# Kernel tuning notes

Measured on AMD Instinct MI355X. Metric: run time of the kernel, lower is better.

The kernel has to match this reference:

```python
import jax, jax.numpy as jnp
import numpy as np
from jax import lax

IN_PLANES = 64
OUT_PLANES = 128
NSAMPLE = 16
BN_EPS = 1e-5


def setup_inputs() -> dict:
    key = jax.random.key(0)
    k1, k2, k3 = jax.random.split(key, 3)
    B, N = 8, 8192
    xyz = jax.random.normal(k1, (B, N, 3), jnp.float32)
    feature = jax.random.normal(k2, (B, N, IN_PLANES), jnp.float32)
    W = jax.random.normal(k3, (OUT_PLANES, IN_PLANES), jnp.float32) * (1.0 / np.sqrt(IN_PLANES))
    gamma = jnp.ones((OUT_PLANES,), jnp.float32)
    beta = jnp.zeros((OUT_PLANES,), jnp.float32)
    return {"xyz": xyz, "feature": feature, "W": W, "gamma": gamma, "beta": beta, "npoint": 2048}


def farthest_point_sample(xyz, npoint):
    # xyz: [B, N, 3] -> centroids: [B, npoint] int32. Deterministic start at index 0
    # (torch version uses a random start; math is otherwise identical).
    B, N, _ = xyz.shape

    def step(carry, _):
        distance, farthest = carry  # [B,N], [B]
        centroid = jnp.take_along_axis(xyz, farthest[:, None, None], axis=1)  # [B,1,3]
        dist = jnp.sum((xyz - centroid) ** 2, axis=-1)  # [B,N]
        distance = jnp.minimum(distance, dist)
        new_far = jnp.argmax(distance, axis=-1).astype(jnp.int32)
        return (distance, new_far), farthest

    init = (jnp.full((B, N), 1e10, xyz.dtype), jnp.zeros((B,), jnp.int32))
    _, cents = lax.scan(step, init, None, length=npoint)  # [npoint, B]
    return cents.T  # [B, npoint]


def knn_point(nsample, xyz, new_xyz):
    # squared pairwise distances [B, M, N], then k smallest
    d = (-2.0 * jnp.einsum('bmc,bnc->bmn', new_xyz, xyz)
         + jnp.sum(new_xyz ** 2, -1)[:, :, None]
         + jnp.sum(xyz ** 2, -1)[:, None, :])
    _, idx = lax.top_k(-d, nsample)  # [B, M, nsample]
    return idx


def _forward(xyz, feature, W, gamma, beta, npoint):
    cent_idx = farthest_point_sample(xyz, npoint)  # [B, npoint]
    new_xyz = jnp.take_along_axis(xyz, cent_idx[:, :, None], axis=1)  # [B, npoint, 3]
    idx = knn_point(NSAMPLE, xyz, new_xyz)  # [B, npoint, K]
    grouped = jax.vmap(lambda f, i: f[i])(feature, idx)  # [B, npoint, K, Cin]
    h = jnp.einsum('bnkc,oc->bnko', grouped, W)  # Linear, bias=False
    # BatchNorm1d over flattened (B*npoint*K, Cout): per-channel batch stats
    m = jnp.mean(h, axis=(0, 1, 2))
    v = jnp.mean((h - m) ** 2, axis=(0, 1, 2))  # biased variance (torch normalization)
    h = (h - m) * lax.rsqrt(v + BN_EPS) * gamma + beta
    h = jax.nn.relu(h)
    new_feature = jnp.max(h, axis=2)  # max-pool over K neighbors
    return new_xyz, new_feature


def reference(xyz, feature, W, gamma, beta, npoint):
    return _forward(xyz, feature, W, gamma, beta, npoint)
```

## Files before the change

kernel.cpp:

```cpp
#include <hip/hip_runtime.h>
#include <stdint.h>

#define NPTS 8192
#define NBATCH 8
#define NPOINT 2048
#define KNN_K 16
#define CIN 64
#define COUT 128

typedef unsigned long long u64;
typedef unsigned int u32;

#define MAXU64(a, b) (((a) > (b)) ? (a) : (b))
#define MAXF64(a, b) fmax((a), (b))

__device__ __forceinline__ double wave_max_f64(double v) {
#define DPPSTEP(C)                                                             \
  {                                                                            \
    u64 k = (u64)__double_as_longlong(v);                                      \
    u32 lo = (u32)k, hi = (u32)(k >> 32);                                      \
    u32 nlo = (u32)__builtin_amdgcn_update_dpp(0, (int)lo, C, 0xf, 0xf, true); \
    u32 nhi = (u32)__builtin_amdgcn_update_dpp(0, (int)hi, C, 0xf, 0xf, true); \
    double o = __longlong_as_double((long long)(((u64)nhi << 32) | nlo));      \
    v = fmax(v, o);                                                            \
  }
  DPPSTEP(0x111)
  DPPSTEP(0x112)
  DPPSTEP(0x114)
  DPPSTEP(0x118)
  DPPSTEP(0x142)
  DPPSTEP(0x143)
#undef DPPSTEP
  return v;
}

__device__ __forceinline__ u64 wave_max_u64(u64 k) {
  u32 lo = (u32)k, hi = (u32)(k >> 32);
#define DPPSTEP(C)                                                             \
  {                                                                            \
    u32 nlo = (u32)__builtin_amdgcn_update_dpp(0, (int)lo, C, 0xf, 0xf, true); \
    u32 nhi = (u32)__builtin_amdgcn_update_dpp(0, (int)hi, C, 0xf, 0xf, true); \
    u64 cur = ((u64)hi << 32) | lo;                                            \
    u64 oth = ((u64)nhi << 32) | nlo;                                          \
    if (oth > cur) { hi = nhi; lo = nlo; }                                     \
  }
  DPPSTEP(0x111)
  DPPSTEP(0x112)
  DPPSTEP(0x114)
  DPPSTEP(0x118)
  DPPSTEP(0x142)
  DPPSTEP(0x143)
#undef DPPSTEP
  return ((u64)hi << 32) | lo;
}

__global__ __launch_bounds__(512) void fps_kernel(const float* __restrict__ xyz,
                                                  int* __restrict__ cent) {
  const int b = blockIdx.x;
  const int tid = threadIdx.x;
  const float* xb = xyz + (size_t)b * NPTS * 3;
  __shared__ float xs[NPTS];
  __shared__ float ys[NPTS];
  __shared__ float zs[NPTS];
  __shared__ __align__(16) double kbuf[2][8];

  float px[16], py[16], pz[16], dist[16];
  u32 klo[16];
#pragma unroll
  for (int j = 0; j < 16; ++j) {
    int i = tid + 512 * j;
    float x = xb[i * 3 + 0], y = xb[i * 3 + 1], z = xb[i * 3 + 2];
    px[j] = x; py[j] = y; pz[j] = z;
    dist[j] = 1e10f;
    xs[i] = x; ys[i] = y; zs[i] = z;
    klo[j] = ~(u32)i;
  }
  if (tid == 0) cent[b * NPOINT] = 0;
  __syncthreads();
  float cx = xs[0], cy = ys[0], cz = zs[0];
  const int lane = tid & 63;
  const int wid = tid >> 6;

  for (int it = 1; it < NPOINT; ++it) {
    double key[16];
#pragma unroll
    for (int j = 0; j < 16; ++j) {
      float dx = px[j] - cx, dy = py[j] - cy, dz = pz[j] - cz;
      float dd = dx * dx + dy * dy + dz * dz;
      float t = fminf(dist[j], dd);
      dist[j] = t;
      key[j] = __longlong_as_double(
          (long long)(((u64)__float_as_uint(t) << 32) | klo[j]));
    }
#pragma unroll
    for (int s = 1; s < 16; s <<= 1) {
#pragma unroll
      for (int j = 0; j < 16; j += 2 * s) key[j] = MAXF64(key[j], key[j + s]);
    }
    double wk = wave_max_f64(key[0]);
    if (lane == 63) kbuf[it & 1][wid] = wk;
    __syncthreads();
    const double2* kb = (const double2*)&kbuf[it & 1][0];
    double2 p0 = kb[0], p1 = kb[1], p2 = kb[2], p3 = kb[3];
    double m0 = MAXF64(p0.x, p0.y), m1 = MAXF64(p1.x, p1.y);
    double m2 = MAXF64(p2.x, p2.y), m3 = MAXF64(p3.x, p3.y);
    double best = MAXF64(MAXF64(m0, m1), MAXF64(m2, m3));
    u32 widx = ~(u32)(u64)__double_as_longlong(best);
    if (tid == 0) cent[b * NPOINT + it] = (int)widx;
    cx = xs[widx]; cy = ys[widx]; cz = zs[widx];
  }
}

__global__ __launch_bounds__(256) void knn_kernel(const float* __restrict__ xyz,
                                                  const int* __restrict__ cent,
                                                  int* __restrict__ knn,
                                                  float* __restrict__ out_xyz) {
  const int pt = blockIdx.x;
  const int b = pt >> 11;
  const int tid = threadIdx.x;
  const float* xb = xyz + (size_t)b * NPTS * 3;
  const int ci = cent[pt];
  const float mx = xb[ci * 3 + 0], my = xb[ci * 3 + 1], mz = xb[ci * 3 + 2];
  if (tid < 3) out_xyz[pt * 3 + tid] = xb[ci * 3 + tid];
  const float sm = mx * mx + my * my + mz * mz;

  float d[32];
  float lv = 3.0e38f;
  int lj = 0;
#pragma unroll
  for (int j = 0; j < 32; ++j) {
    int i = tid + 256 * j;
    float x = xb[i * 3 + 0], y = xb[i * 3 + 1], z = xb[i * 3 + 2];
    float dot = mx * x + my * y + mz * z;
    float sp = x * x + y * y + z * z;
    float dd = -2.0f * dot + sm + sp;
    d[j] = dd;
    if (dd < lv) { lv = dd; lj = j; }
  }

  __shared__ __align__(16) u64 kbuf[2][4];
  const int lane = tid & 63;

  for (int p = 0; p < KNN_K; ++p) {
    u32 fb = __float_as_uint(lv);
    u32 mapped = (fb & 0x80000000u) ? ~fb : (fb | 0x80000000u);
    u32 idx = (u32)(tid + (lj << 8));
    u64 ik = ~(((u64)mapped << 32) | (u64)idx);
    u64 wk = wave_max_u64(ik);
    if (lane == 63) kbuf[p & 1][tid >> 6] = wk;
    __syncthreads();
    const ulonglong2* kb = (const ulonglong2*)&kbuf[p & 1][0];
    ulonglong2 q0 = kb[0], q1 = kb[1];
    u64 best = MAXU64(MAXU64(q0.x, q0.y), MAXU64(q1.x, q1.y));
    u32 widx = (u32)(~best);
    if (tid == 0) knn[pt * KNN_K + p] = (int)widx;
    if (tid == (int)(widx & 255u)) {
      int j0 = (int)(widx >> 8);
      float nlv = 3.0e38f;
      int nlj = 0;
#pragma unroll
      for (int j = 0; j < 32; ++j) {
        if (j == j0) d[j] = 3.0e38f;
        if (d[j] < nlv) { nlv = d[j]; nlj = j; }
      }
      lv = nlv; lj = nlj;
    }
  }
}

__global__ __launch_bounds__(256) void gemm_stats_kernel(const float* __restrict__ feat,
                                                         const float* __restrict__ W,
                                                         const int* __restrict__ knn,
                                                         float* __restrict__ part,
                                                         float* __restrict__ mxbuf,
                                                         float* __restrict__ mnbuf) {
  const int tid = threadIdx.x;
  const int o0 = (tid & 63) * 2;
  const int o1 = o0 + 1;
  const int grp = tid >> 6;
  __shared__ __align__(16) float g[128][CIN];
  __shared__ int kidx[128];
  __shared__ float sred[4][128];

  const int rowbase = blockIdx.x * 128;
  if (tid < 128) kidx[tid] = knn[rowbase + tid];

  float4 w0v[16], w1v[16];
  {
    const float4* wv0 = (const float4*)(W + (size_t)o0 * CIN);
    const float4* wv1 = (const float4*)(W + (size_t)o1 * CIN);
#pragma unroll
    for (int q = 0; q < 16; ++q) { w0v[q] = wv0[q]; w1v[q] = wv1[q]; }
  }
  __syncthreads();
#pragma unroll
  for (int s = 0; s < 8; ++s) {
    int v = tid + 256 * s;
    int row = v >> 4, q = v & 15;
    int gr = rowbase + row;
    int bb = gr >> 15;
    const float4* src = (const float4*)(feat + (size_t)(bb * NPTS + kidx[row]) * CIN);
    *((float4*)&g[row][q * 4]) = src[q];
  }
  __syncthreads();

  float s1_0 = 0.f, s2_0 = 0.f, s1_1 = 0.f, s2_1 = 0.f;
#pragma unroll
  for (int pp = 0; pp < 2; ++pp) {
    const int ptl = grp + pp * 4;
    float mx0 = -3.0e38f, mn0 = 3.0e38f, mx1 = -3.0e38f, mn1 = 3.0e38f;
#pragma unroll
    for (int k = 0; k < KNN_K; ++k) {
      const int row = ptl * 16 + k;
      float a0 = 0.f, a1 = 0.f;
#pragma unroll
      for (int q = 0; q < 16; ++q) {
        float4 a = *((const float4*)&g[row][q * 4]);
        a0 += w0v[q].x * a.x + w0v[q].y * a.y + w0v[q].z * a.z + w0v[q].w * a.w;
        a1 += w1v[q].x * a.x + w1v[q].y * a.y + w1v[q].z * a.z + w1v[q].w * a.w;
      }
      s1_0 += a0; s2_0 += a0 * a0; mx0 = fmaxf(mx0, a0); mn0 = fminf(mn0, a0);
      s1_1 += a1; s2_1 += a1 * a1; mx1 = fmaxf(mx1, a1); mn1 = fminf(mn1, a1);
    }
    const size_t pt = (size_t)blockIdx.x * 8 + ptl;
    mxbuf[pt * COUT + o0] = mx0;
    mxbuf[pt * COUT + o1] = mx1;
    mnbuf[pt * COUT + o0] = mn0;
    mnbuf[pt * COUT + o1] = mn1;
  }
  sred[grp][o0] = s1_0; sred[grp][o1] = s1_1;
  __syncthreads();
  if (tid < 128) {
    float t = sred[0][tid] + sred[1][tid] + sred[2][tid] + sred[3][tid];
    part[blockIdx.x * 256 + tid] = t;
  }
  __syncthreads();
  sred[grp][o0] = s2_0; sred[grp][o1] = s2_1;
  __syncthreads();
  if (tid < 128) {
    float t = sred[0][tid] + sred[1][tid] + sred[2][tid] + sred[3][tid];
    part[blockIdx.x * 256 + 128 + tid] = t;
  }
}

__global__ __launch_bounds__(256) void bn_reduce_kernel(const float* __restrict__ part,
                                                        const float* __restrict__ gamma,
                                                        const float* __restrict__ beta,
                                                        float* __restrict__ stats) {
  const int o = blockIdx.x;
  const int tid = threadIdx.x;
  float s1 = 0.f, s2 = 0.f;
  for (int p = tid; p < 2048; p += 256) {
    s1 += part[p * 256 + o];
    s2 += part[p * 256 + 128 + o];
  }
  __shared__ float r1[256], r2[256];
  r1[tid] = s1; r2[tid] = s2;
  __syncthreads();
  for (int s = 128; s >= 1; s >>= 1) {
    if (tid < s) { r1[tid] += r1[tid + s]; r2[tid] += r2[tid + s]; }
    __syncthreads();
  }
  if (tid == 0) {
    const float n = (float)(NBATCH * NPOINT * KNN_K);
    float mean = r1[0] / n;
    float var = r2[0] / n - mean * mean;
    float inv = rsqrtf(var + 1e-5f);
    float sc = gamma[o] * inv;
    stats[o] = sc;
    stats[128 + o] = beta[o] - mean * sc;
  }
}

__global__ __launch_bounds__(256) void finalize_kernel(float* __restrict__ out_feat,
                                                       const float* __restrict__ mnbuf,
                                                       const float* __restrict__ stats) {
  const int i = blockIdx.x * 256 + threadIdx.x;
  const int o = i & 127;
  const float sc = stats[o];
  const float sh = stats[128 + o];
  const float mx = out_feat[i];
  const float mn = mnbuf[i];
  const float sel = (sc >= 0.f) ? mx : mn;
  out_feat[i] = fmaxf(sel * sc + sh, 0.f);
}

extern "C" void kernel_launch(void* const* d_in, const int* in_sizes, int n_in,
                              void* d_out, int out_size, void* d_ws, size_t ws_size,
                              hipStream_t stream) {
  const float* xyz = (const float*)d_in[0];
  const float* feat = (const float*)d_in[1];
  const float* W = (const float*)d_in[2];
  const float* gamma = (const float*)d_in[3];
  const float* beta = (const float*)d_in[4];
  float* out = (float*)d_out;

  int* cent = (int*)d_ws;
  int* knn = cent + NBATCH * NPOINT;
  float* part = (float*)(knn + NBATCH * NPOINT * KNN_K);
  float* stats = part + 2048 * 256;
  float* mnbuf = stats + 256;

  float* out_xyz = out;
  float* out_feat = out + NBATCH * NPOINT * 3;

  hipLaunchKernelGGL(fps_kernel, dim3(NBATCH), dim3(512), 0, stream, xyz, cent);
  hipLaunchKernelGGL(knn_kernel, dim3(NBATCH * NPOINT), dim3(256), 0, stream,
                     xyz, cent, knn, out_xyz);
  hipLaunchKernelGGL(gemm_stats_kernel, dim3(2048), dim3(256), 0, stream,
                     feat, W, knn, part, out_feat, mnbuf);
  hipLaunchKernelGGL(bn_reduce_kernel, dim3(128), dim3(256), 0, stream,
                     part, gamma, beta, stats);
  hipLaunchKernelGGL(finalize_kernel, dim3(8192), dim3(256), 0, stream,
                     out_feat, mnbuf, stats);
}
```

Before: 2.047 ms.

## Sort FPS points by octant per wave and skip waves via bounding-box bound

```diff
diff --git a/kernel.cpp b/kernel.cpp
--- a/kernel.cpp
+++ b/kernel.cpp
@@ -62,42 +62,113 @@
   __shared__ float xs[NPTS];
   __shared__ float ys[NPTS];
   __shared__ float zs[NPTS];
+  __shared__ unsigned short sorted[NPTS];
+  __shared__ int cnt8[8], base8[8], cur8[8];
+  __shared__ float bbox[8][6];
+  __shared__ float scratch[512][6];
   __shared__ __align__(16) double kbuf[2][8];
+
+  if (tid < 8) { cnt8[tid] = 0; cur8[tid] = 0; }
+
+  float lx[16], ly[16], lz[16];
+#pragma unroll
+  for (int j = 0; j < 16; ++j) {
+    int i = tid + 512 * j;
+    lx[j] = xb[i * 3 + 0];
+    ly[j] = xb[i * 3 + 1];
+    lz[j] = xb[i * 3 + 2];
+  }
+  __syncthreads();
+#pragma unroll
+  for (int j = 0; j < 16; ++j) {
+    int i = tid + 512 * j;
+    xs[i] = lx[j]; ys[i] = ly[j]; zs[i] = lz[j];
+    int oct = ((lx[j] > 0.f) ? 4 : 0) | ((ly[j] > 0.f) ? 2 : 0) | ((lz[j] > 0.f) ? 1 : 0);
+    atomicAdd(&cnt8[oct], 1);
+  }
+  __syncthreads();
+  if (tid == 0) {
+    int acc = 0;
+#pragma unroll
+    for (int o = 0; o < 8; ++o) { base8[o] = acc; acc += cnt8[o]; }
+  }
+  __syncthreads();
+#pragma unroll
+  for (int j = 0; j < 16; ++j) {
+    int i = tid + 512 * j;
+    int oct = ((lx[j] > 0.f) ? 4 : 0) | ((ly[j] > 0.f) ? 2 : 0) | ((lz[j] > 0.f) ? 1 : 0);
+    int pos = base8[oct] + atomicAdd(&cur8[oct], 1);
+    sorted[pos] = (unsigned short)i;
+  }
+  if (tid == 0) cent[b * NPOINT] = 0;
+  __syncthreads();
+
+  const int lane = tid & 63;
+  const int wid = tid >> 6;
 
   float px[16], py[16], pz[16], dist[16];
   u32 klo[16];
+  float xl = 3e38f, xh = -3e38f, yl = 3e38f, yh = -3e38f, zl = 3e38f, zh = -3e38f;
 #pragma unroll
   for (int j = 0; j < 16; ++j) {
-    int i = tid + 512 * j;
-    float x = xb[i * 3 + 0], y = xb[i * 3 + 1], z = xb[i * 3 + 2];
+    int pi = (int)sorted[wid * 1024 + lane + 64 * j];
+    float x = xs[pi], y = ys[pi], z = zs[pi];
     px[j] = x; py[j] = y; pz[j] = z;
     dist[j] = 1e10f;
-    xs[i] = x; ys[i] = y; zs[i] = z;
-    klo[j] = ~(u32)i;
-  }
-  if (tid == 0) cent[b * NPOINT] = 0;
-  __syncthreads();
+    klo[j] = ~(u32)pi;
+    xl = fminf(xl, x); xh = fmaxf(xh, x);
+    yl = fminf(yl, y); yh = fmaxf(yh, y);
+    zl = fminf(zl, z); zh = fmaxf(zh, z);
+  }
+  scratch[tid][0] = xl; scratch[tid][1] = xh;
+  scratch[tid][2] = yl; scratch[tid][3] = yh;
+  scratch[tid][4] = zl; scratch[tid][5] = zh;
+  __syncthreads();
+  if (tid < 48) {
+    int w = tid / 6, q = tid % 6;
+    float v = scratch[w * 64][q];
+    if (q & 1) { for (int l = 1; l < 64; ++l) v = fmaxf(v, scratch[w * 64 + l][q]); }
+    else       { for (int l = 1; l < 64; ++l) v = fminf(v, scratch[w * 64 + l][q]); }
+    bbox[w][q] = v;
+  }
+  __syncthreads();
+  const float bx0 = bbox[wid][0], bx1 = bbox[wid][1];
+  const float by0 = bbox[wid][2], by1 = bbox[wid][3];
+  const float bz0 = bbox[wid][4], bz1 = bbox[wid][5];
+
   float cx = xs[0], cy = ys[0], cz = zs[0];
-  const int lane = tid & 63;
-  const int wid = tid >> 6;
+  float dmax = 1e10f;
+  double prev_wk = 0.0;
 
   for (int it = 1; it < NPOINT; ++it) {
-    double key[16];
-#pragma unroll
-    for (int j = 0; j < 16; ++j) {
-      float dx = px[j] - cx, dy = py[j] - cy, dz = pz[j] - cz;
-      float dd = dx * dx + dy * dy + dz * dz;
-      float t = fminf(dist[j], dd);
-      dist[j] = t;
-      key[j] = __longlong_as_double(
-          (long long)(((u64)__float_as_uint(t) << 32) | klo[j]));
+    float ax = fmaxf(fmaxf(bx0 - cx, cx - bx1), 0.f);
+    float ay = fmaxf(fmaxf(by0 - cy, cy - by1), 0.f);
+    float az = fmaxf(fmaxf(bz0 - cz, cz - bz1), 0.f);
+    float LB = ax * ax + ay * ay + az * az;
+    int skip = (LB > dmax * 1.00002f) ? 1 : 0;
+    skip = __builtin_amdgcn_readfirstlane(skip);
+    double wk;
+    if (skip) {
+      wk = prev_wk;
+    } else {
+      double key[16];
+#pragma unroll
+      for (int j = 0; j < 16; ++j) {
+        float dx = px[j] - cx, dy = py[j] - cy, dz = pz[j] - cz;
+        float dd = dx * dx + dy * dy + dz * dz;
+        float t = fminf(dist[j], dd);
+        dist[j] = t;
+        key[j] = __longlong_as_double(
+            (long long)(((u64)__float_as_uint(t) << 32) | klo[j]));
+      }
+#pragma unroll
+      for (int s = 1; s < 16; s <<= 1) {
+#pragma unroll
+        for (int j = 0; j < 16; j += 2 * s) key[j] = MAXF64(key[j], key[j + s]);
+      }
+      wk = wave_max_f64(key[0]);
+      prev_wk = wk;
     }
-#pragma unroll
-    for (int s = 1; s < 16; s <<= 1) {
-#pragma unroll
-      for (int j = 0; j < 16; j += 2 * s) key[j] = MAXF64(key[j], key[j + s]);
-    }
-    double wk = wave_max_f64(key[0]);
     if (lane == 63) kbuf[it & 1][wid] = wk;
     __syncthreads();
     const double2* kb = (const double2*)&kbuf[it & 1][0];
@@ -108,6 +179,8 @@
     u32 widx = ~(u32)(u64)__double_as_longlong(best);
     if (tid == 0) cent[b * NPOINT + it] = (int)widx;
     cx = xs[widx]; cy = ys[widx]; cz = zs[widx];
+    u64 ob = (u64)__double_as_longlong(kbuf[it & 1][wid]);
+    dmax = __uint_as_float((u32)(ob >> 32));
   }
 }
 
```

Result: faster. 2.002 ms (-2.2%).

## Morton-sort FPS points into chunks and skip chunks via bounding-box bounds

Applied to the files above, without the earlier changes.

```diff
diff --git a/kernel.cpp b/kernel.cpp
--- a/kernel.cpp
+++ b/kernel.cpp
@@ -54,61 +54,212 @@
   return ((u64)hi << 32) | lo;
 }
 
+__device__ __forceinline__ float wave_min_f32(float v) {
+#define STEP(C)                                                                \
+  {                                                                            \
+    int o = __builtin_amdgcn_update_dpp((int)__float_as_uint(v),               \
+                                        (int)__float_as_uint(v), C, 0xf, 0xf,  \
+                                        false);                                \
+    v = fminf(v, __uint_as_float((u32)o));                                     \
+  }
+  STEP(0x111) STEP(0x112) STEP(0x114) STEP(0x118) STEP(0x142) STEP(0x143)
+#undef STEP
+  return v;
+}
+__device__ __forceinline__ float wave_max_f32(float v) {
+#define STEP(C)                                                                \
+  {                                                                            \
+    int o = __builtin_amdgcn_update_dpp((int)__float_as_uint(v),               \
+                                        (int)__float_as_uint(v), C, 0xf, 0xf,  \
+                                        false);                                \
+    v = fmaxf(v, __uint_as_float((u32)o));                                     \
+  }
+  STEP(0x111) STEP(0x112) STEP(0x114) STEP(0x118) STEP(0x142) STEP(0x143)
+#undef STEP
+  return v;
+}
+
+__device__ __forceinline__ u32 spread3(u32 v) {
+  return (v & 1u) | ((v & 2u) << 2) | ((v & 4u) << 4) | ((v & 8u) << 6);
+}
+
 __global__ __launch_bounds__(512) void fps_kernel(const float* __restrict__ xyz,
                                                   int* __restrict__ cent) {
   const int b = blockIdx.x;
   const int tid = threadIdx.x;
+  const int lane = tid & 63;
+  const int wid = tid >> 6;
   const float* xb = xyz + (size_t)b * NPTS * 3;
-  __shared__ float xs[NPTS];
-  __shared__ float ys[NPTS];
-  __shared__ float zs[NPTS];
-  __shared__ __align__(16) double kbuf[2][8];
-
-  float px[16], py[16], pz[16], dist[16];
-  u32 klo[16];
+
+  __shared__ float X[NPTS], Y[NPTS], Z[NPTS];
+  __shared__ float Dd[NPTS];
+  __shared__ unsigned short O[NPTS];
+  __shared__ __align__(16) float bboxT[6][128];
+  __shared__ __align__(16) float khiT[128];
+  __shared__ __align__(16) u64 keys[128];
+  __shared__ float gred[8][6];
+  __shared__ int t8[8];
+  __shared__ int p0s;
+  u32* cnt = (u32*)Dd;
+  u32* tsum = ((u32*)Dd) + 4096;
+
+  float lx[16], ly[16], lz[16];
+  float gxl = 3e38f, gxh = -3e38f, gyl = 3e38f, gyh = -3e38f, gzl = 3e38f, gzh = -3e38f;
 #pragma unroll
   for (int j = 0; j < 16; ++j) {
     int i = tid + 512 * j;
     float x = xb[i * 3 + 0], y = xb[i * 3 + 1], z = xb[i * 3 + 2];
-    px[j] = x; py[j] = y; pz[j] = z;
-    dist[j] = 1e10f;
-    xs[i] = x; ys[i] = y; zs[i] = z;
-    klo[j] = ~(u32)i;
+    lx[j] = x; ly[j] = y; lz[j] = z;
+    gxl = fminf(gxl, x); gxh = fmaxf(gxh, x);
+    gyl = fminf(gyl, y); gyh = fmaxf(gyh, y);
+    gzl = fminf(gzl, z); gzh = fmaxf(gzh, z);
+  }
+  gxl = wave_min_f32(gxl); gxh = wave_max_f32(gxh);
+  gyl = wave_min_f32(gyl); gyh = wave_max_f32(gyh);
+  gzl = wave_min_f32(gzl); gzh = wave_max_f32(gzh);
+  if (lane == 63) {
+    gred[wid][0] = gxl; gred[wid][1] = gxh; gred[wid][2] = gyl;
+    gred[wid][3] = gyh; gred[wid][4] = gzl; gred[wid][5] = gzh;
+  }
+  __syncthreads();
+  float gx0 = gred[0][0], gx1 = gred[0][1], gy0 = gred[0][2];
+  float gy1 = gred[0][3], gz0 = gred[0][4], gz1 = gred[0][5];
+#pragma unroll
+  for (int w = 1; w < 8; ++w) {
+    gx0 = fminf(gx0, gred[w][0]); gx1 = fmaxf(gx1, gred[w][1]);
+    gy0 = fminf(gy0, gred[w][2]); gy1 = fmaxf(gy1, gred[w][3]);
+    gz0 = fminf(gz0, gred[w][4]); gz1 = fmaxf(gz1, gred[w][5]);
+  }
+  const float sx = 16.f / fmaxf((gx1 - gx0) * 1.0001f, 1e-20f);
+  const float sy = 16.f / fmaxf((gy1 - gy0) * 1.0001f, 1e-20f);
+  const float sz = 16.f / fmaxf((gz1 - gz0) * 1.0001f, 1e-20f);
+#pragma unroll
+  for (int k = 0; k < 8; ++k) cnt[tid * 8 + k] = 0;
+  __syncthreads();
+
+  u32 mc[16];
+#pragma unroll
+  for (int j = 0; j < 16; ++j) {
+    int qx = min(15, max(0, (int)((lx[j] - gx0) * sx)));
+    int qy = min(15, max(0, (int)((ly[j] - gy0) * sy)));
+    int qz = min(15, max(0, (int)((lz[j] - gz0) * sz)));
+    mc[j] = (spread3((u32)qx) << 2) | (spread3((u32)qy) << 1) | spread3((u32)qz);
+    atomicAdd(&cnt[mc[j]], 1);
+  }
+  __syncthreads();
+  {
+    u32 s = 0;
+#pragma unroll
+    for (int k = 0; k < 8; ++k) { u32 c = cnt[tid * 8 + k]; cnt[tid * 8 + k] = s; s += c; }
+    tsum[tid] = s;
+  }
+  __syncthreads();
+  if (tid < 8) {
+    u32 s = 0;
+    for (int k = 0; k < 64; ++k) { u32 c = tsum[tid * 64 + k]; tsum[tid * 64 + k] = s; s += c; }
+    t8[tid] = (int)s;
+  }
+  __syncthreads();
+  if (tid == 0) {
+    int s = 0;
+#pragma unroll
+    for (int k = 0; k < 8; ++k) { int c = t8[k]; t8[k] = s; s += c; }
+  }
+  __syncthreads();
+  {
+    u32 base = tsum[tid] + (u32)t8[tid >> 6];
+#pragma unroll
+    for (int k = 0; k < 8; ++k) cnt[tid * 8 + k] += base;
+  }
+  __syncthreads();
+#pragma unroll
+  for (int j = 0; j < 16; ++j) {
+    int i = tid + 512 * j;
+    u32 pos = atomicAdd(&cnt[mc[j]], 1);
+    X[pos] = lx[j]; Y[pos] = ly[j]; Z[pos] = lz[j];
+    O[pos] = (unsigned short)i;
+    if (i == 0) p0s = (int)pos;
   }
   if (tid == 0) cent[b * NPOINT] = 0;
   __syncthreads();
-  float cx = xs[0], cy = ys[0], cz = zs[0];
-  const int lane = tid & 63;
-  const int wid = tid >> 6;
+  for (int r = 0; r < 16; ++r) {
+    int c = wid * 16 + r;
+    int p = c * 64 + lane;
+    float x = X[p], y = Y[p], z = Z[p];
+    float xl = wave_min_f32(x), xh = wave_max_f32(x);
+    float yl = wave_min_f32(y), yh = wave_max_f32(y);
+    float zl = wave_min_f32(z), zh = wave_max_f32(z);
+    if (lane == 63) {
+      bboxT[0][c] = xl; bboxT[1][c] = xh; bboxT[2][c] = yl;
+      bboxT[3][c] = yh; bboxT[4][c] = zl; bboxT[5][c] = zh;
+    }
+  }
+#pragma unroll
+  for (int j = 0; j < 16; ++j) Dd[tid + 512 * j] = 1e10f;
+  if (tid < 128) {
+    khiT[tid] = 1e10f;
+    keys[tid] = ((u64)__float_as_uint(1e10f) << 32);
+  }
+  __syncthreads();
+
+  float cx = X[p0s], cy = Y[p0s], cz = Z[p0s];
+
+#define PROCESS_CHUNK(c)                                                       \
+  {                                                                            \
+    int p = (c)*64 + lane;                                                     \
+    float x = X[p], y = Y[p], z = Z[p];                                        \
+    float dc = Dd[p];                                                          \
+    u32 o = (u32)O[p];                                                         \
+    float dx = x - cx, dy = y - cy, dz = z - cz;                               \
+    float dd = dx * dx + dy * dy + dz * dz;       \
+    float t = fminf(dc, dd);                                                   \
+    Dd[p] = t;                                                                 \
+    u32 klo = ((8191u - o) << 13) | (u32)p;                                    \
+    double k = __longlong_as_double(                                           \
+        (long long)(((u64)__float_as_uint(t) << 32) | klo));                   \
+    k = wave_max_f64(k);                                                       \
+    if (lane == 63) {                                                          \
+      u64 kb = (u64)__double_as_longlong(k);                                   \
+      keys[c] = kb;                                                            \
+      khiT[c] = __uint_as_float((u32)(kb >> 32));                              \
+    }                                                                          \
+  }
 
   for (int it = 1; it < NPOINT; ++it) {
-    double key[16];
-#pragma unroll
-    for (int j = 0; j < 16; ++j) {
-      float dx = px[j] - cx, dy = py[j] - cy, dz = pz[j] - cz;
-      float dd = dx * dx + dy * dy + dz * dz;
-      float t = fminf(dist[j], dd);
-      dist[j] = t;
-      key[j] = __longlong_as_double(
-          (long long)(((u64)__float_as_uint(t) << 32) | klo[j]));
-    }
-#pragma unroll
-    for (int s = 1; s < 16; s <<= 1) {
-#pragma unroll
-      for (int j = 0; j < 16; j += 2 * s) key[j] = MAXF64(key[j], key[j + s]);
-    }
-    double wk = wave_max_f64(key[0]);
-    if (lane == 63) kbuf[it & 1][wid] = wk;
+    const int c0 = 2 * lane;
+    float2 bxl = *(const float2*)&bboxT[0][c0];
+    float2 bxh = *(const float2*)&bboxT[1][c0];
+    float2 byl = *(const float2*)&bboxT[2][c0];
+    float2 byh = *(const float2*)&bboxT[3][c0];
+    float2 bzl = *(const float2*)&bboxT[4][c0];
+    float2 bzh = *(const float2*)&bboxT[5][c0];
+    float2 kh = *(const float2*)&khiT[c0];
+    float ax = fmaxf(fmaxf(bxl.x - cx, cx - bxh.x), 0.f);
+    float ay = fmaxf(fmaxf(byl.x - cy, cy - byh.x), 0.f);
+    float az = fmaxf(fmaxf(bzl.x - cz, cz - bzh.x), 0.f);
+    float LB0 = ax * ax + ay * ay + az * az;
+    ax = fmaxf(fmaxf(bxl.y - cx, cx - bxh.y), 0.f);
+    ay = fmaxf(fmaxf(byl.y - cy, cy - byh.y), 0.f);
+    az = fmaxf(fmaxf(bzl.y - cz, cz - bzh.y), 0.f);
+    float LB1 = ax * ax + ay * ay + az * az;
+    bool mine0 = !(LB0 > kh.x * 1.00002f) && ((c0 & 7) == wid);
+    bool mine1 = !(LB1 > kh.y * 1.00002f) && (((c0 + 1) & 7) == wid);
+    u64 mA = __ballot(mine0);
+    u64 mB = __ballot(mine1);
     __syncthreads();
-    const double2* kb = (const double2*)&kbuf[it & 1][0];
-    double2 p0 = kb[0], p1 = kb[1], p2 = kb[2], p3 = kb[3];
-    double m0 = MAXF64(p0.x, p0.y), m1 = MAXF64(p1.x, p1.y);
-    double m2 = MAXF64(p2.x, p2.y), m3 = MAXF64(p3.x, p3.y);
-    double best = MAXF64(MAXF64(m0, m1), MAXF64(m2, m3));
-    u32 widx = ~(u32)(u64)__double_as_longlong(best);
-    if (tid == 0) cent[b * NPOINT + it] = (int)widx;
-    cx = xs[widx]; cy = ys[widx]; cz = zs[widx];
-  }
+    while (mA) { int l2 = __ffsll(mA) - 1; mA &= mA - 1; PROCESS_CHUNK(2 * l2); }
+    while (mB) { int l2 = __ffsll(mB) - 1; mB &= mB - 1; PROCESS_CHUNK(2 * l2 + 1); }
+    __syncthreads();
+    double2 kk = *(const double2*)&keys[c0];
+    double mk = MAXF64(kk.x, kk.y);
+    mk = wave_max_f64(mk);
+    u32 lo = (u32)(u64)__double_as_longlong(mk);
+    lo = (u32)__builtin_amdgcn_readlane((int)lo, 63);
+    u32 pos = lo & 8191u;
+    if (tid == 0) cent[b * NPOINT + it] = (int)(8191u - ((lo >> 13) & 8191u));
+    cx = X[pos]; cy = Y[pos]; cz = Z[pos];
+  }
+#undef PROCESS_CHUNK
 }
 
 __global__ __launch_bounds__(256) void knn_kernel(const float* __restrict__ xyz,
```

Result: slower. 2.745 ms (+34.1%).

## Spatially bin points per wave in FPS and skip waves via bounding-box bound

Applied to the files above, without the earlier changes.

```diff
diff --git a/kernel.cpp b/kernel.cpp
--- a/kernel.cpp
+++ b/kernel.cpp
@@ -34,6 +34,24 @@
   return v;
 }
 
+__device__ __forceinline__ double row16_max_f64(double v) {
+#define DPPSTEP(C)                                                             \
+  {                                                                            \
+    u64 k = (u64)__double_as_longlong(v);                                      \
+    u32 lo = (u32)k, hi = (u32)(k >> 32);                                      \
+    u32 nlo = (u32)__builtin_amdgcn_update_dpp(0, (int)lo, C, 0xf, 0xf, true); \
+    u32 nhi = (u32)__builtin_amdgcn_update_dpp(0, (int)hi, C, 0xf, 0xf, true); \
+    double o = __longlong_as_double((long long)(((u64)nhi << 32) | nlo));      \
+    v = fmax(v, o);                                                            \
+  }
+  DPPSTEP(0x111)
+  DPPSTEP(0x112)
+  DPPSTEP(0x114)
+  DPPSTEP(0x118)
+#undef DPPSTEP
+  return v;
+}
+
 __device__ __forceinline__ u64 wave_max_u64(u64 k) {
   u32 lo = (u32)k, hi = (u32)(k >> 32);
 #define DPPSTEP(C)                                                             \
@@ -54,60 +72,171 @@
   return ((u64)hi << 32) | lo;
 }
 
-__global__ __launch_bounds__(512) void fps_kernel(const float* __restrict__ xyz,
-                                                  int* __restrict__ cent) {
+__device__ __forceinline__ float wave_min_f32(float v) {
+#define STEP(C)                                                                \
+  {                                                                            \
+    int o = __builtin_amdgcn_update_dpp((int)__float_as_uint(v),               \
+                                        (int)__float_as_uint(v), C, 0xf, 0xf,  \
+                                        false);                                \
+    v = fminf(v, __uint_as_float((u32)o));                                     \
+  }
+  STEP(0x111) STEP(0x112) STEP(0x114) STEP(0x118) STEP(0x142) STEP(0x143)
+#undef STEP
+  return v;
+}
+__device__ __forceinline__ float wave_max_f32(float v) {
+#define STEP(C)                                                                \
+  {                                                                            \
+    int o = __builtin_amdgcn_update_dpp((int)__float_as_uint(v),               \
+                                        (int)__float_as_uint(v), C, 0xf, 0xf,  \
+                                        false);                                \
+    v = fmaxf(v, __uint_as_float((u32)o));                                     \
+  }
+  STEP(0x111) STEP(0x112) STEP(0x114) STEP(0x118) STEP(0x142) STEP(0x143)
+#undef STEP
+  return v;
+}
+
+__device__ __forceinline__ float bcast63(float v) {
+  return __uint_as_float(
+      (u32)__builtin_amdgcn_readlane((int)__float_as_uint(v), 63));
+}
+
+__global__ __launch_bounds__(1024) void fps_kernel(const float* __restrict__ xyz,
+                                                   int* __restrict__ cent) {
   const int b = blockIdx.x;
   const int tid = threadIdx.x;
+  const int lane = tid & 63;
+  const int wid = tid >> 6;
   const float* xb = xyz + (size_t)b * NPTS * 3;
-  __shared__ float xs[NPTS];
-  __shared__ float ys[NPTS];
-  __shared__ float zs[NPTS];
-  __shared__ __align__(16) double kbuf[2][8];
-
-  float px[16], py[16], pz[16], dist[16];
-  u32 klo[16];
-#pragma unroll
-  for (int j = 0; j < 16; ++j) {
-    int i = tid + 512 * j;
+
+  __shared__ float X[NPTS], Y[NPTS], Z[NPTS];
+  __shared__ unsigned short O[NPTS];
+  __shared__ float gred[16][6];
+  __shared__ int cnt16[16], base16[16], cur16[16];
+  __shared__ __align__(16) u64 kbuf[2][16];
+
+  float lx[8], ly[8], lz[8];
+  float xl = 3e38f, xh = -3e38f, yl = 3e38f, yh = -3e38f, zl = 3e38f, zh = -3e38f;
+#pragma unroll
+  for (int j = 0; j < 8; ++j) {
+    int i = tid + 1024 * j;
     float x = xb[i * 3 + 0], y = xb[i * 3 + 1], z = xb[i * 3 + 2];
+    lx[j] = x; ly[j] = y; lz[j] = z;
+    xl = fminf(xl, x); xh = fmaxf(xh, x);
+    yl = fminf(yl, y); yh = fmaxf(yh, y);
+    zl = fminf(zl, z); zh = fmaxf(zh, z);
+  }
+  xl = wave_min_f32(xl); xh = wave_max_f32(xh);
+  yl = wave_min_f32(yl); yh = wave_max_f32(yh);
+  zl = wave_min_f32(zl); zh = wave_max_f32(zh);
+  if (lane == 63) {
+    gred[wid][0] = xl; gred[wid][1] = xh; gred[wid][2] = yl;
+    gred[wid][3] = yh; gred[wid][4] = zl; gred[wid][5] = zh;
+  }
+  if (tid < 16) { cnt16[tid] = 0; cur16[tid] = 0; }
+  __syncthreads();
+  float gx0 = gred[0][0], gx1 = gred[0][1], gy0 = gred[0][2];
+  float gy1 = gred[0][3], gz0 = gred[0][4], gz1 = gred[0][5];
+#pragma unroll
+  for (int w = 1; w < 16; ++w) {
+    gx0 = fminf(gx0, gred[w][0]); gx1 = fmaxf(gx1, gred[w][1]);
+    gy0 = fminf(gy0, gred[w][2]); gy1 = fmaxf(gy1, gred[w][3]);
+    gz0 = fminf(gz0, gred[w][4]); gz1 = fmaxf(gz1, gred[w][5]);
+  }
+  const float sx = 4.f / fmaxf((gx1 - gx0) * 1.0001f, 1e-20f);
+  const float sy = 2.f / fmaxf((gy1 - gy0) * 1.0001f, 1e-20f);
+  const float sz = 2.f / fmaxf((gz1 - gz0) * 1.0001f, 1e-20f);
+
+  int bin[8];
+#pragma unroll
+  for (int j = 0; j < 8; ++j) {
+    int qx = min(3, max(0, (int)((lx[j] - gx0) * sx)));
+    int qy = min(1, max(0, (int)((ly[j] - gy0) * sy)));
+    int qz = min(1, max(0, (int)((lz[j] - gz0) * sz)));
+    bin[j] = (qx << 2) | (qy << 1) | qz;
+    atomicAdd(&cnt16[bin[j]], 1);
+  }
+  __syncthreads();
+  if (tid == 0) {
+    int s = 0;
+#pragma unroll
+    for (int k = 0; k < 16; ++k) { base16[k] = s; s += cnt16[k]; }
+  }
+  __syncthreads();
+#pragma unroll
+  for (int j = 0; j < 8; ++j) {
+    int i = tid + 1024 * j;
+    int pos = base16[bin[j]] + atomicAdd(&cur16[bin[j]], 1);
+    X[pos] = lx[j]; Y[pos] = ly[j]; Z[pos] = lz[j];
+    O[pos] = (unsigned short)i;
+  }
+  if (tid == 0) cent[b * NPOINT] = 0;
+  __syncthreads();
+
+  float px[8], py[8], pz[8], dist[8];
+  u32 klo[8];
+  float bxl = 3e38f, bxh = -3e38f, byl = 3e38f, byh = -3e38f, bzl = 3e38f, bzh = -3e38f;
+#pragma unroll
+  for (int j = 0; j < 8; ++j) {
+    int p = wid * 512 + lane + 64 * j;
+    float x = X[p], y = Y[p], z = Z[p];
+    u32 orig = (u32)O[p];
     px[j] = x; py[j] = y; pz[j] = z;
     dist[j] = 1e10f;
-    xs[i] = x; ys[i] = y; zs[i] = z;
-    klo[j] = ~(u32)i;
-  }
-  if (tid == 0) cent[b * NPOINT] = 0;
-  __syncthreads();
-  float cx = xs[0], cy = ys[0], cz = zs[0];
-  const int lane = tid & 63;
-  const int wid = tid >> 6;
+    klo[j] = ((8191u - orig) << 13) | (u32)p;
+    bxl = fminf(bxl, x); bxh = fmaxf(bxh, x);
+    byl = fminf(byl, y); byh = fmaxf(byh, y);
+    bzl = fminf(bzl, z); bzh = fmaxf(bzh, z);
+  }
+  const float bx0 = bcast63(wave_min_f32(bxl)), bx1 = bcast63(wave_max_f32(bxh));
+  const float by0 = bcast63(wave_min_f32(byl)), by1 = bcast63(wave_max_f32(byh));
+  const float bz0 = bcast63(wave_min_f32(bzl)), bz1 = bcast63(wave_max_f32(bzh));
+
+  float cx = xb[0], cy = xb[1], cz = xb[2];
+  float dmax = 1e10f;
+  double prev_wk = 0.0;
 
   for (int it = 1; it < NPOINT; ++it) {
-    double key[16];
-#pragma unroll
-    for (int j = 0; j < 16; ++j) {
-      float dx = px[j] - cx, dy = py[j] - cy, dz = pz[j] - cz;
-      float dd = dx * dx + dy * dy + dz * dz;
-      float t = fminf(dist[j], dd);
-      dist[j] = t;
-      key[j] = __longlong_as_double(
-          (long long)(((u64)__float_as_uint(t) << 32) | klo[j]));
+    float ax = fmaxf(fmaxf(bx0 - cx, cx - bx1), 0.f);
+    float ay = fmaxf(fmaxf(by0 - cy, cy - by1), 0.f);
+    float az = fmaxf(fmaxf(bz0 - cz, cz - bz1), 0.f);
+    float LB = ax * ax + ay * ay + az * az;
+    int skip = (LB > dmax * 1.00002f) ? 1 : 0;
+    skip = __builtin_amdgcn_readfirstlane(skip);
+    double wk;
+    if (skip) {
+      wk = prev_wk;
+    } else {
+      double key[8];
+#pragma unroll
+      for (int j = 0; j < 8; ++j) {
+        float dx = px[j] - cx, dy = py[j] - cy, dz = pz[j] - cz;
+        float dd = dx * dx + dy * dy + dz * dz;
+        float t = fminf(dist[j], dd);
+        dist[j] = t;
+        key[j] = __longlong_as_double(
+            (long long)(((u64)__float_as_uint(t) << 32) | klo[j]));
+      }
+#pragma unroll
+      for (int s = 1; s < 8; s <<= 1) {
+#pragma unroll
+        for (int j = 0; j < 8; j += 2 * s) key[j] = MAXF64(key[j], key[j + s]);
+      }
+      wk = wave_max_f64(key[0]);
+      prev_wk = wk;
     }
-#pragma unroll
-    for (int s = 1; s < 16; s <<= 1) {
-#pragma unroll
-      for (int j = 0; j < 16; j += 2 * s) key[j] = MAXF64(key[j], key[j + s]);
-    }
-    double wk = wave_max_f64(key[0]);
-    if (lane == 63) kbuf[it & 1][wid] = wk;
+    if (lane == 63) kbuf[it & 1][wid] = (u64)__double_as_longlong(wk);
+    dmax = __uint_as_float((u32)__builtin_amdgcn_readlane(
+        (int)(u32)(((u64)__double_as_longlong(wk)) >> 32), 63));
     __syncthreads();
-    const double2* kb = (const double2*)&kbuf[it & 1][0];
-    double2 p0 = kb[0], p1 = kb[1], p2 = kb[2], p3 = kb[3];
-    double m0 = MAXF64(p0.x, p0.y), m1 = MAXF64(p1.x, p1.y);
-    double m2 = MAXF64(p2.x, p2.y), m3 = MAXF64(p3.x, p3.y);
-    double best = MAXF64(MAXF64(m0, m1), MAXF64(m2, m3));
-    u32 widx = ~(u32)(u64)__double_as_longlong(best);
-    if (tid == 0) cent[b * NPOINT + it] = (int)widx;
-    cx = xs[widx]; cy = ys[widx]; cz = zs[widx];
+    double kv = __longlong_as_double((long long)kbuf[it & 1][lane & 15]);
+    kv = row16_max_f64(kv);
+    u32 rlo = (u32)__builtin_amdgcn_readlane(
+        (int)(u32)(u64)__double_as_longlong(kv), 15);
+    u32 pos = rlo & 8191u;
+    if (tid == 0) cent[b * NPOINT + it] = (int)(8191u - ((rlo >> 13) & 8191u));
+    cx = X[pos]; cy = Y[pos]; cz = Z[pos];
   }
 }
 
@@ -304,7 +433,7 @@
   float* out_xyz = out;
   float* out_feat = out + NBATCH * NPOINT * 3;
 
-  hipLaunchKernelGGL(fps_kernel, dim3(NBATCH), dim3(512), 0, stream, xyz, cent);
+  hipLaunchKernelGGL(fps_kernel, dim3(NBATCH), dim3(1024), 0, stream, xyz, cent);
   hipLaunchKernelGGL(knn_kernel, dim3(NBATCH * NPOINT), dim3(256), 0, stream,
                      xyz, cent, knn, out_xyz);
   hipLaunchKernelGGL(gemm_stats_kernel, dim3(2048), dim3(256), 0, stream,
```

Result: slower. 2.147 ms (+4.9%).
